# Optimization experiments

Measured on AMD Instinct MI355X. Metric: run time of the kernel, lower is better.

## Reference

```python
import jax, jax.numpy as jnp
import numpy as np

N = 8192
IN_DIM = 512
OUT_DIM = 512


def setup_inputs() -> dict:
    key = jax.random.key(0)
    kA, kX, k1, k2, k3, k4 = jax.random.split(key, 6)
    A = jax.random.uniform(kA, (N, N), dtype=jnp.float32)  # strictly positive -> nonzero triu
    X = jax.random.normal(kX, (N, IN_DIM), dtype=jnp.float32)
    s = 1.0 / np.sqrt(IN_DIM)
    W1 = jax.random.uniform(k1, (OUT_DIM, IN_DIM), minval=-s, maxval=s, dtype=jnp.float32)  # fc
    b1 = jax.random.uniform(k2, (OUT_DIM,), minval=-s, maxval=s, dtype=jnp.float32)
    W2 = jax.random.uniform(k3, (OUT_DIM, IN_DIM), minval=-s, maxval=s, dtype=jnp.float32)  # fc2
    b2 = jax.random.uniform(k4, (OUT_DIM,), minval=-s, maxval=s, dtype=jnp.float32)
    return {"A": A, "X": X, "W1": W1, "b1": b1, "W2": W2, "b2": b2}


def reference(A, X, W1, b1, W2, b2):
    n = A.shape[0]
    # strictly upper-triangular mask (diagonal=1); with uniform(0,1) fill all these
    # entries are nonzero, so torch.nonzero selects exactly them: m = n(n-1)/2 values.
    triu_mask = jnp.triu(jnp.ones((n, n), dtype=bool), k=1)
    m = n * (n - 1) // 2
    # torch.median = lower median = sorted[(m-1)//2]; pad non-triu entries with +inf
    vals = jnp.where(triu_mask, A, jnp.inf).reshape(-1)
    median_value = jnp.sort(vals)[(m - 1) // 2]
    # A[A < median] = 0
    A_thr = jnp.where(A < median_value, jnp.zeros((), A.dtype), A)
    A_norm = jax.nn.softmax(A_thr, axis=-1)
    fcX = X @ W1.T + b1    # [N, out_dim]
    fc2X = X @ W2.T + b2   # [N, out_dim]
    out = jax.nn.leaky_relu(0.1 * fc2X + 0.9 * (A_norm @ fcX), negative_slope=0.01)
    return out
```

## Files before the change

kernel.cpp:

```cpp
#include <hip/hip_runtime.h>

#define DEVI __device__ __forceinline__

typedef __attribute__((ext_vector_type(8))) short short8;
typedef __attribute__((ext_vector_type(4))) float f32x4;

static constexpr int NN = 8192;
static constexpr int DD = 512;
static constexpr unsigned LOB = 0x3EFE0000u;
static constexpr unsigned HIB = 0x3F020000u;
static constexpr long long K_RANK = 16775167LL;

static constexpr size_t WS_HIST   = 0;
static constexpr size_t WS_CNT    = 1048576;
static constexpr size_t WS_MED    = 1048832;
static constexpr size_t WS_COARSE = 1049088;
static constexpr size_t WS_XB     = 2097152;
static constexpr size_t WS_W1B  = WS_XB  + (size_t)NN * DD * 2;
static constexpr size_t WS_W2B  = WS_W1B + (size_t)DD * DD * 2;
static constexpr size_t WS_FCXT = WS_W2B + (size_t)DD * DD * 2;
static constexpr size_t WS_FC2  = WS_FCXT + (size_t)NN * DD * 2;
static constexpr size_t WS_UP   = WS_FC2 + (size_t)NN * DD * 4;
static constexpr size_t WS_ZP   = WS_UP  + (size_t)4 * NN * DD * 2;

DEVI unsigned short f2bf(float f) {
  unsigned u = __float_as_uint(f);
  u += 0x7fffu + ((u >> 16) & 1u);
  return (unsigned short)(u >> 16);
}
DEVI float bf2f(unsigned short h) { return __uint_as_float(((unsigned)h) << 16); }
DEVI int swz(int row, int kq) { return kq ^ ((row >> 1) & 3); }

DEVI void gl_lds16(const void* g, void* l) {
  __builtin_amdgcn_global_load_lds(
      (const __attribute__((address_space(1))) unsigned*)g,
      (__attribute__((address_space(3))) unsigned*)l, 16, 0, 0);
}

#define VMCNT(n) asm volatile("s_waitcnt vmcnt(" #n ")" ::: "memory")
#define LGKM0 asm volatile("s_waitcnt lgkmcnt(0)" ::: "memory")

__global__ __launch_bounds__(256) void zero_k(uint4* __restrict__ hist4,
                                              unsigned* __restrict__ cntmed) {
  hist4[blockIdx.x * 256 + threadIdx.x] = (uint4){0u, 0u, 0u, 0u};
  if (blockIdx.x == 0 && threadIdx.x < 2) cntmed[threadIdx.x * 64] = 0u;
}


DEVI void convert_body(const float* __restrict__ X, const float* __restrict__ W1,
                       const float* __restrict__ W2, unsigned short* __restrict__ Xb,
                       unsigned short* __restrict__ W1b, unsigned short* __restrict__ W2b,
                       int cb, int tid) {
  const long long NX = (long long)NN * DD;
  const long long NW = (long long)DD * DD;
  const long long total4 = (NX + 2 * NW) / 4;
  for (long long q = (long long)cb * 512 + tid; q < total4; q += 65536LL) {
    long long e = q << 2;
    const float4* src; unsigned short* dst; long long off;
    if (e < NX)           { src = (const float4*)X;  dst = Xb;  off = e; }
    else if (e < NX + NW) { src = (const float4*)W1; dst = W1b; off = e - NX; }
    else                  { src = (const float4*)W2; dst = W2b; off = e - NX - NW; }
    float4 v = src[off >> 2];
    ushort4 o;
    o.x = f2bf(v.x); o.y = f2bf(v.y); o.z = f2bf(v.z); o.w = f2bf(v.w);
    *(ushort4*)(dst + off) = o;
  }
}

DEVI void hist_body(const float* __restrict__ A, unsigned* __restrict__ hist,
                    unsigned* __restrict__ below, int hb, int tid) {
  unsigned cnt = 0;
  const float4* A4 = (const float4*)A;
  const long long STR = 458752LL;
#pragma unroll 1
  for (long long q0 = (long long)hb * 512 + tid; q0 < 16777216LL; q0 += 8 * STR) {
    float4 v[8];
    int act = 0;
#pragma unroll
    for (int i = 0; i < 8; ++i) {
      long long qi = q0 + i * STR;
      if (qi < 16777216LL) {
        int row = (int)(qi >> 11);
        int col = (int)((qi & 2047) << 2);
        if (col + 3 > row) { act |= 1 << i; v[i] = A4[qi]; }
      }
    }
#pragma unroll
    for (int i = 0; i < 8; ++i) {
      if (act & (1 << i)) {
        long long qi = q0 + i * STR;
        int row = (int)(qi >> 11);
        int col = (int)((qi & 2047) << 2);
        float vv[4] = {v[i].x, v[i].y, v[i].z, v[i].w};
#pragma unroll
        for (int j = 0; j < 4; ++j) {
          if (col + j > row) {
            unsigned u = __float_as_uint(vv[j]);
            if (u < LOB) cnt++;
            else if (u < HIB) atomicAdd(&hist[u - LOB], 1u);
          }
        }
      }
    }
  }
  for (int off = 32; off > 0; off >>= 1) cnt += __shfl_down(cnt, off);
  if ((tid & 63) == 0 && cnt) atomicAdd(below, cnt);
}

__global__ __launch_bounds__(512) void stage1_k(const float* __restrict__ A,
                                                const float* __restrict__ X,
                                                const float* __restrict__ W1,
                                                const float* __restrict__ W2,
                                                unsigned* __restrict__ hist,
                                                unsigned* __restrict__ below,
                                                unsigned short* __restrict__ Xb,
                                                unsigned short* __restrict__ W1b,
                                                unsigned short* __restrict__ W2b) {
  const int bx = blockIdx.x;
  if (bx < 128) convert_body(X, W1, W2, Xb, W1b, W2b, bx, threadIdx.x);
  else          hist_body(A, hist, below, bx - 128, threadIdx.x);
}


template <bool BROW, bool OBF>
DEVI void gemm_small_body(const unsigned short* __restrict__ Am,
                          const unsigned short* __restrict__ Bm,
                          const float* __restrict__ bias, void* __restrict__ outp,
                          int ldout, int m0, int n0, char* apB, char* btB) {
  const int tid = threadIdx.x, lane = tid & 63, w = tid >> 6;
  const int wm = w >> 2, wn = w & 3;
  const int lr = lane & 15, lq = lane >> 4;
  const int rL = lane >> 2, kq = lane & 3;
  f32x4 acc[2][4];
#pragma unroll
  for (int i = 0; i < 2; ++i)
#pragma unroll
    for (int j = 0; j < 4; ++j) acc[i][j] = (f32x4){0.f, 0.f, 0.f, 0.f};

#pragma unroll 1
  for (int kt = 0; kt < 16; ++kt) {
    const int k0 = kt * 32;
    __syncthreads();
    if (w < 4) {
      int r = w * 16 + rL;
      gl_lds16(Am + ((size_t)(m0 + r) * DD + k0 + swz(r, kq) * 8), apB + w * 1024);
    }
#pragma unroll
    for (int i = 0; i < 2; ++i) {
      int blk = w * 2 + i;
      int r = blk * 16 + rL;
      gl_lds16(Bm + ((size_t)(n0 + r) * DD + k0 + swz(r, kq) * 8), btB + blk * 1024);
    }
    __syncthreads();
    short8 a[2], b[4];
#pragma unroll
    for (int fr = 0; fr < 2; ++fr) {
      int r = wm * 32 + fr * 16 + lr;
      a[fr] = *(const short8*)(apB + r * 64 + swz(r, lq) * 16);
    }
#pragma unroll
    for (int fc = 0; fc < 4; ++fc) {
      int r = wn * 64 + fc * 16 + lr;
      b[fc] = *(const short8*)(btB + r * 64 + swz(r, lq) * 16);
    }
#pragma unroll
    for (int fr = 0; fr < 2; ++fr)
#pragma unroll
      for (int fc = 0; fc < 4; ++fc)
        acc[fr][fc] = __builtin_amdgcn_mfma_f32_16x16x32_bf16(a[fr], b[fc], acc[fr][fc], 0, 0, 0);
  }
#pragma unroll
  for (int fr = 0; fr < 2; ++fr)
#pragma unroll
    for (int fc = 0; fc < 4; ++fc)
#pragma unroll
      for (int j = 0; j < 4; ++j) {
        int row = m0 + wm * 32 + fr * 16 + lq * 4 + j;
        int col = n0 + wn * 64 + fc * 16 + lr;
        float v = acc[fr][fc][j] + (BROW ? bias[row] : bias[col]);
        if (OBF) ((unsigned short*)outp)[(size_t)row * ldout + col] = f2bf(v);
        else     ((float*)outp)[(size_t)row * ldout + col] = v;
      }
}

__global__ __launch_bounds__(512, 2) void stage2_k(const unsigned short* __restrict__ Xb,
                                                   const unsigned short* __restrict__ W1b,
                                                   const unsigned short* __restrict__ W2b,
                                                   const float* __restrict__ b1,
                                                   const float* __restrict__ b2,
                                                   unsigned short* __restrict__ fcXT,
                                                   float* __restrict__ fc2) {
  __shared__ alignas(16) char plds[20480];
  const int bx = blockIdx.x;
  if (bx < 256) {
    int m0 = ((bx >> 3) & 7) * 64;
    int n0 = ((bx & 7) | ((bx >> 6) << 3)) * 256;
    gemm_small_body<true, true>(W1b, Xb, b1, (void*)fcXT, NN, m0, n0, plds, plds + 4096);
  } else {
    int q = bx - 256;
    gemm_small_body<false, false>(Xb, W2b, b2, (void*)fc2, DD,
                                  (q >> 1) * 64, (q & 1) * 256, plds, plds + 4096);
  }
}

__global__ __launch_bounds__(256) void coarse_k(const unsigned* __restrict__ hist,
                                                unsigned* __restrict__ coarse) {
  __shared__ unsigned part[4];
  unsigned v = hist[blockIdx.x * 256 + threadIdx.x];
  for (int off = 32; off > 0; off >>= 1) v += __shfl_down(v, off);
  if ((threadIdx.x & 63) == 0) part[threadIdx.x >> 6] = v;
  __syncthreads();
  if (threadIdx.x == 0) coarse[blockIdx.x] = part[0] + part[1] + part[2] + part[3];
}

__global__ __launch_bounds__(1024) void select_k(const unsigned* __restrict__ hist,
                                                 const unsigned* __restrict__ coarse,
                                                 const unsigned* __restrict__ below,
                                                 unsigned* __restrict__ med) {
  __shared__ unsigned ssum[1024];
  __shared__ int owner;
  __shared__ unsigned tg_s;
  const int t = threadIdx.x;
  unsigned own = coarse[t];
  ssum[t] = own;
  __syncthreads();
  for (int off = 1; off < 1024; off <<= 1) {
    unsigned v = (t >= off) ? ssum[t - off] : 0u;
    __syncthreads();
    ssum[t] += v;
    __syncthreads();
  }
  long long target = K_RANK - (long long)(*below);
  unsigned incl = ssum[t];
  unsigned excl = incl - own;
  if (target >= (long long)excl && target < (long long)incl) {
    owner = t;
    tg_s = (unsigned)(target - (long long)excl);
  }
  __syncthreads();
  const int to = owner;
  const unsigned tg = tg_s;
  unsigned v256 = (t < 256) ? hist[to * 256 + t] : 0u;
  __syncthreads();
  if (t < 256) ssum[t] = v256;
  __syncthreads();
  for (int off = 1; off < 256; off <<= 1) {
    unsigned v = (t < 256 && t >= off) ? ssum[t - off] : 0u;
    __syncthreads();
    if (t < 256) ssum[t] += v;
    __syncthreads();
  }
  if (t < 256) {
    unsigned incl2 = ssum[t];
    unsigned excl2 = incl2 - v256;
    if (tg >= excl2 && tg < incl2) *med = LOB + (unsigned)(to * 256 + t);
  }
}

static constexpr int LDS_A0 = 0;
static constexpr int LDS_A1 = 8192;
static constexpr int LDS_B0 = 16384;
static constexpr int LDS_B1 = 49152;

__global__ __launch_bounds__(512, 2) void main_gemm_k(const float* __restrict__ A,
                                                      const unsigned short* __restrict__ fcXT,
                                                      const unsigned* __restrict__ medp,
                                                      unsigned short* __restrict__ Up,
                                                      float* __restrict__ Zp) {
  __shared__ alignas(16) char lds[81920];
  const int tid = threadIdx.x, lane = tid & 63, w = tid >> 6;
  const int wm = w >> 2, wn = w & 3;
  const int lr = lane & 15, lq = lane >> 4;
  const int fid = blockIdx.x;
  const int xcd = fid & 7;
  const int ks = xcd >> 1;
  const int m0 = (((xcd & 1) << 5) | (fid >> 3)) << 7;
  const int kbase = ks * 2048;
  const float med = __uint_as_float(*medp);
  const int rB = lane >> 2, kqB = lane & 3;
  const int rA = tid >> 2, cqA = tid & 3;
  const float* aRow = A + (size_t)(m0 + rA) * NN;
  const int ldsAw = rA * 64 + swz(rA, cqA) * 16;

  float zacc = 0.f;
  f32x4 acc[4][8];
#pragma unroll
  for (int i = 0; i < 4; ++i)
#pragma unroll
    for (int j = 0; j < 8; ++j) acc[i][j] = (f32x4){0.f, 0.f, 0.f, 0.f};
  float4 vA00, vA01, vA10, vA11;

#define CONV8(V0, V1, DST)                                                     \
  {                                                                            \
    float vv[8] = {V0.x, V0.y, V0.z, V0.w, V1.x, V1.y, V1.z, V1.w};            \
    short8 pb;                                                                 \
    _Pragma("unroll")                                                          \
    for (int j = 0; j < 8; ++j) {                                              \
      float a_ = vv[j];                                                        \
      float p_ = (a_ < med) ? 1.0f : __expf(a_);                               \
      unsigned short h_ = f2bf(p_);                                            \
      pb[j] = (short)h_;                                                       \
      zacc += bf2f(h_);                                                        \
    }                                                                          \
    *(short8*)(DST) = pb;                                                      \
  }

  {
#pragma unroll
    for (int i = 0; i < 4; ++i) {
      int blk = w * 4 + i;
      int o = blk * 16 + rB;
      gl_lds16(fcXT + ((size_t)o * NN + kbase + swz(o, kqB) * 8), lds + LDS_B0 + blk * 1024);
    }
    const float* ap0 = aRow + kbase + cqA * 8;
    float4 t0 = *(const float4*)ap0;
    float4 t1 = *(const float4*)(ap0 + 4);
    vA00 = *(const float4*)(ap0 + 32);
    vA01 = *(const float4*)(ap0 + 36);
    CONV8(t0, t1, lds + LDS_A0 + ldsAw);
  }
  __syncthreads();

#define ITER(KT, CUR, NCUR, VAC0, VAC1, VAN0, VAN1)                            \
  {                                                                            \
    const int kt_ = (KT);                                                      \
    if (kt_ < 63) {                                                            \
      const int k1 = kbase + (kt_ + 1) * 32;                                   \
      _Pragma("unroll")                                                        \
      for (int i = 0; i < 4; ++i) {                                            \
        int blk = w * 4 + i;                                                   \
        int o = blk * 16 + rB;                                                 \
        gl_lds16(fcXT + ((size_t)o * NN + k1 + swz(o, kqB) * 8),               \
                 lds + LDS_B##NCUR + blk * 1024);                              \
      }                                                                        \
      if (kt_ < 62) {                                                          \
        const float* apf = aRow + kbase + (kt_ + 2) * 32 + cqA * 8;            \
        asm volatile("global_load_dwordx4 %0, %2, off\n\t"                     \
                     "global_load_dwordx4 %1, %2, off offset:16"               \
                     : "=&v"(VAN0), "=&v"(VAN1)                                \
                     : "v"(apf)                                                \
                     : "memory");                                              \
      }                                                                        \
    }                                                                          \
    short8 af[4], bfr[8];                                                      \
    _Pragma("unroll")                                                          \
    for (int fr = 0; fr < 4; ++fr) {                                           \
      int r = wm * 64 + fr * 16 + lr;                                          \
      af[fr] = *(const short8*)(lds + LDS_A##CUR + r * 64 + swz(r, lq) * 16);  \
    }                                                                          \
    _Pragma("unroll")                                                          \
    for (int fc = 0; fc < 8; ++fc) {                                           \
      int o = wn * 128 + fc * 16 + lr;                                         \
      bfr[fc] = *(const short8*)(lds + LDS_B##CUR + o * 64 + swz(o, lq) * 16); \
    }                                                                          \
    __builtin_amdgcn_s_setprio(1);                                             \
    _Pragma("unroll")                                                          \
    for (int fr = 0; fr < 4; ++fr)                                             \
      _Pragma("unroll")                                                        \
      for (int fc = 0; fc < 8; ++fc)                                           \
        acc[fr][fc] = __builtin_amdgcn_mfma_f32_16x16x32_bf16(af[fr], bfr[fc], \
                                                              acc[fr][fc], 0, 0, 0); \
    __builtin_amdgcn_s_setprio(0);                                             \
    if (kt_ < 63) {                                                            \
      if (kt_ < 62) { VMCNT(6); } else { VMCNT(4); }                           \
      __builtin_amdgcn_sched_barrier(0);                                       \
      CONV8(VAC0, VAC1, lds + LDS_A##NCUR + ldsAw);                            \
      if (kt_ < 62) { VMCNT(2); } else { VMCNT(0); }                           \
      LGKM0;                                                                   \
      __builtin_amdgcn_s_barrier();                                            \
    }                                                                          \
  }

#pragma unroll 1
  for (int t2 = 0; t2 < 32; ++t2) {
    ITER(2 * t2,     0, 1, vA00, vA01, vA10, vA11);
    ITER(2 * t2 + 1, 1, 0, vA10, vA11, vA00, vA01);
  }
#undef ITER
#undef CONV8

  zacc += __shfl_xor(zacc, 1);
  zacc += __shfl_xor(zacc, 2);
  if ((lane & 3) == 0) Zp[(size_t)ks * NN + m0 + rA] = zacc;
#pragma unroll
  for (int fr = 0; fr < 4; ++fr)
#pragma unroll
    for (int fc = 0; fc < 8; ++fc)
#pragma unroll
      for (int j = 0; j < 4; ++j) {
        int row = m0 + wm * 64 + fr * 16 + lq * 4 + j;
        int col = wn * 128 + fc * 16 + lr;
        Up[((size_t)ks << 22) + ((size_t)row << 9) + col] = f2bf(acc[fr][fc][j]);
      }
}

__global__ __launch_bounds__(256) void reduce_k(const unsigned short* __restrict__ Up,
                                                const float* __restrict__ Zp,
                                                const float* __restrict__ fc2,
                                                float* __restrict__ out) {
  long long t = (long long)blockIdx.x * blockDim.x + threadIdx.x;
  if (t >= (long long)NN * DD / 8) return;
  long long base = t << 3;
  int row = (int)(base >> 9);
  float Z = Zp[row] + Zp[NN + row] + Zp[2 * NN + row] + Zp[3 * NN + row];
  float inv = 0.9f / Z;
  float s[8] = {0, 0, 0, 0, 0, 0, 0, 0};
#pragma unroll
  for (int sp = 0; sp < 4; ++sp) {
    const uint4 u = *(const uint4*)(Up + ((long long)sp << 22) + base);
    const unsigned uu[4] = {u.x, u.y, u.z, u.w};
#pragma unroll
    for (int j = 0; j < 4; ++j) {
      s[2 * j]     += __uint_as_float(uu[j] << 16);
      s[2 * j + 1] += __uint_as_float(uu[j] & 0xffff0000u);
    }
  }
  float4 fa = *(const float4*)(fc2 + base);
  float4 fb = *(const float4*)(fc2 + base + 4);
  float fv[8] = {fa.x, fa.y, fa.z, fa.w, fb.x, fb.y, fb.z, fb.w};
  float o[8];
#pragma unroll
  for (int j = 0; j < 8; ++j) {
    float v = 0.1f * fv[j] + inv * s[j];
    o[j] = v >= 0.f ? v : 0.01f * v;
  }
  *(float4*)(out + base)     = (float4){o[0], o[1], o[2], o[3]};
  *(float4*)(out + base + 4) = (float4){o[4], o[5], o[6], o[7]};
}

extern "C" void kernel_launch(void* const* d_in, const int* in_sizes, int n_in,
                              void* d_out, int out_size, void* d_ws, size_t ws_size,
                              hipStream_t stream) {
  const float* A  = (const float*)d_in[0];
  const float* X  = (const float*)d_in[1];
  const float* W1 = (const float*)d_in[2];
  const float* b1 = (const float*)d_in[3];
  const float* W2 = (const float*)d_in[4];
  const float* b2 = (const float*)d_in[5];
  char* ws = (char*)d_ws;
  unsigned* hist   = (unsigned*)(ws + WS_HIST);
  unsigned* cnt    = (unsigned*)(ws + WS_CNT);
  unsigned* med    = (unsigned*)(ws + WS_MED);
  unsigned* coarse = (unsigned*)(ws + WS_COARSE);
  unsigned short* Xb   = (unsigned short*)(ws + WS_XB);
  unsigned short* W1b  = (unsigned short*)(ws + WS_W1B);
  unsigned short* W2b  = (unsigned short*)(ws + WS_W2B);
  unsigned short* fcXT = (unsigned short*)(ws + WS_FCXT);
  float* fc2           = (float*)(ws + WS_FC2);
  unsigned short* Upp  = (unsigned short*)(ws + WS_UP);
  float* Zp            = (float*)(ws + WS_ZP);

  hipLaunchKernelGGL(zero_k, dim3(256), dim3(256), 0, stream, (uint4*)hist, cnt);
  hipLaunchKernelGGL(stage1_k, dim3(1024), dim3(512), 0, stream,
                     A, X, W1, W2, hist, cnt, Xb, W1b, W2b);
  hipLaunchKernelGGL(coarse_k, dim3(1024), dim3(256), 0, stream, hist, coarse);
  hipLaunchKernelGGL(select_k, dim3(1), dim3(1024), 0, stream, hist, coarse, cnt, med);
  hipLaunchKernelGGL(stage2_k, dim3(512), dim3(512), 0, stream,
                     Xb, W1b, W2b, b1, b2, fcXT, fc2);
  hipLaunchKernelGGL(main_gemm_k, dim3(256), dim3(512), 0, stream, A, fcXT, med, Upp, Zp);
  hipLaunchKernelGGL(reduce_k, dim3(2048), dim3(256), 0, stream, Upp, Zp, fc2, (float*)d_out);
}
```

Before: 238.9 us.

## Fuse histogram zeroing with conversion, and histogram pass with small GEMMs

Folds the histogram-zeroing kernel into the bf16 conversion kernel, then runs the triangular histogram pass in the same launch as the two small projection GEMMs instead of alongside the conversion. The histogram stride is changed to match the new 1024 histogram blocks. The aim is to drop one launch and overlap the memory-bound histogram scan of A with the compute-bound small GEMMs. The risk is that the histogram blocks and the GEMM blocks (launch bounds 512,2 with shared memory) compete for occupancy, and the GEMM kernel's register limit now also constrains the histogram path.

```diff
diff --git a/kernel.cpp b/kernel.cpp
--- a/kernel.cpp
+++ b/kernel.cpp
@@ -39,12 +39,6 @@
 
 #define VMCNT(n) asm volatile("s_waitcnt vmcnt(" #n ")" ::: "memory")
 #define LGKM0 asm volatile("s_waitcnt lgkmcnt(0)" ::: "memory")
-
-__global__ __launch_bounds__(256) void zero_k(uint4* __restrict__ hist4,
-                                              unsigned* __restrict__ cntmed) {
-  hist4[blockIdx.x * 256 + threadIdx.x] = (uint4){0u, 0u, 0u, 0u};
-  if (blockIdx.x == 0 && threadIdx.x < 2) cntmed[threadIdx.x * 64] = 0u;
-}
 
 
 DEVI void convert_body(const float* __restrict__ X, const float* __restrict__ W1,
@@ -67,11 +61,29 @@
   }
 }
 
+__global__ __launch_bounds__(512) void fused0_k(const float* __restrict__ X,
+                                                const float* __restrict__ W1,
+                                                const float* __restrict__ W2,
+                                                unsigned short* __restrict__ Xb,
+                                                unsigned short* __restrict__ W1b,
+                                                unsigned short* __restrict__ W2b,
+                                                uint4* __restrict__ hist4,
+                                                unsigned* __restrict__ cntmed) {
+  const int bx = blockIdx.x;
+  if (bx < 128) {
+    convert_body(X, W1, W2, Xb, W1b, W2b, bx, threadIdx.x);
+  } else {
+    hist4[(bx - 128) * 512 + threadIdx.x] = (uint4){0u, 0u, 0u, 0u};
+    if (bx == 128 && threadIdx.x < 2) cntmed[threadIdx.x * 64] = 0u;
+  }
+}
+
+
 DEVI void hist_body(const float* __restrict__ A, unsigned* __restrict__ hist,
                     unsigned* __restrict__ below, int hb, int tid) {
   unsigned cnt = 0;
   const float4* A4 = (const float4*)A;
-  const long long STR = 458752LL;
+  const long long STR = 524288LL;
 #pragma unroll 1
   for (long long q0 = (long long)hb * 512 + tid; q0 < 16777216LL; q0 += 8 * STR) {
     float4 v[8];
@@ -106,21 +118,6 @@
   for (int off = 32; off > 0; off >>= 1) cnt += __shfl_down(cnt, off);
   if ((tid & 63) == 0 && cnt) atomicAdd(below, cnt);
 }
-
-__global__ __launch_bounds__(512) void stage1_k(const float* __restrict__ A,
-                                                const float* __restrict__ X,
-                                                const float* __restrict__ W1,
-                                                const float* __restrict__ W2,
-                                                unsigned* __restrict__ hist,
-                                                unsigned* __restrict__ below,
-                                                unsigned short* __restrict__ Xb,
-                                                unsigned short* __restrict__ W1b,
-                                                unsigned short* __restrict__ W2b) {
-  const int bx = blockIdx.x;
-  if (bx < 128) convert_body(X, W1, W2, Xb, W1b, W2b, bx, threadIdx.x);
-  else          hist_body(A, hist, below, bx - 128, threadIdx.x);
-}
-
 
 template <bool BROW, bool OBF>
 DEVI void gemm_small_body(const unsigned short* __restrict__ Am,
@@ -183,23 +180,28 @@
       }
 }
 
-__global__ __launch_bounds__(512, 2) void stage2_k(const unsigned short* __restrict__ Xb,
+__global__ __launch_bounds__(512, 2) void fused1_k(const float* __restrict__ A,
+                                                   const unsigned short* __restrict__ Xb,
                                                    const unsigned short* __restrict__ W1b,
                                                    const unsigned short* __restrict__ W2b,
                                                    const float* __restrict__ b1,
                                                    const float* __restrict__ b2,
                                                    unsigned short* __restrict__ fcXT,
-                                                   float* __restrict__ fc2) {
+                                                   float* __restrict__ fc2,
+                                                   unsigned* __restrict__ hist,
+                                                   unsigned* __restrict__ below) {
   __shared__ alignas(16) char plds[20480];
   const int bx = blockIdx.x;
   if (bx < 256) {
     int m0 = ((bx >> 3) & 7) * 64;
     int n0 = ((bx & 7) | ((bx >> 6) << 3)) * 256;
     gemm_small_body<true, true>(W1b, Xb, b1, (void*)fcXT, NN, m0, n0, plds, plds + 4096);
-  } else {
+  } else if (bx < 512) {
     int q = bx - 256;
     gemm_small_body<false, false>(Xb, W2b, b2, (void*)fc2, DD,
                                   (q >> 1) * 64, (q & 1) * 256, plds, plds + 4096);
+  } else {
+    hist_body(A, hist, below, bx - 512, threadIdx.x);
   }
 }
 
@@ -450,13 +452,12 @@
   unsigned short* Upp  = (unsigned short*)(ws + WS_UP);
   float* Zp            = (float*)(ws + WS_ZP);
 
-  hipLaunchKernelGGL(zero_k, dim3(256), dim3(256), 0, stream, (uint4*)hist, cnt);
-  hipLaunchKernelGGL(stage1_k, dim3(1024), dim3(512), 0, stream,
-                     A, X, W1, W2, hist, cnt, Xb, W1b, W2b);
+  hipLaunchKernelGGL(fused0_k, dim3(256), dim3(512), 0, stream,
+                     X, W1, W2, Xb, W1b, W2b, (uint4*)hist, cnt);
+  hipLaunchKernelGGL(fused1_k, dim3(1536), dim3(512), 0, stream,
+                     A, Xb, W1b, W2b, b1, b2, fcXT, fc2, hist, cnt);
   hipLaunchKernelGGL(coarse_k, dim3(1024), dim3(256), 0, stream, hist, coarse);
   hipLaunchKernelGGL(select_k, dim3(1), dim3(1024), 0, stream, hist, coarse, cnt, med);
-  hipLaunchKernelGGL(stage2_k, dim3(512), dim3(512), 0, stream,
-                     Xb, W1b, W2b, b1, b2, fcXT, fc2);
   hipLaunchKernelGGL(main_gemm_k, dim3(256), dim3(512), 0, stream, A, fcXT, med, Upp, Zp);
   hipLaunchKernelGGL(reduce_k, dim3(2048), dim3(256), 0, stream, Upp, Zp, fc2, (float*)d_out);
 }
```

New measurement: 267.8 us. 1.12x slower.
